# Kernel tuning notes

Hardware: AMD Instinct MI355X
Metric: run time of the kernel (lower is better)

The kernel has to match this reference:

```python
import jax, jax.numpy as jnp
import numpy as np

B, N, I, H = 4, 325, 64, 128
LN_EPS = 1e-5

def setup_inputs() -> dict:
    key = jax.random.key(0)
    ks = jax.random.split(key, 20)
    x = jax.random.normal(ks[0], (B, N, I), dtype=jnp.float32)
    # sparse binary adjacency with self-loops (as the module masks adj == 0)
    a = (jax.random.uniform(ks[1], (B, N, N)) < 0.05).astype(jnp.float32)
    adj = jnp.maximum(a, jnp.eye(N, dtype=jnp.float32)[None])
    h = jax.random.normal(ks[2], (B, N, H), dtype=jnp.float32)
    c = jax.random.normal(ks[3], (B, N, H), dtype=jnp.float32)
    def glorot(k, shape):
        fan_in, fan_out = shape[-1], shape[0]
        s = jnp.sqrt(2.0 / (fan_in + fan_out)).astype(jnp.float32)
        return jax.random.normal(k, shape, dtype=jnp.float32) * s
    params = {
        'W_ih': glorot(ks[4], (4 * H, I)),
        'W_hh': glorot(ks[5], (4 * H, H)),
        'b_ih': jnp.zeros((4 * H,), jnp.float32),
        'b_hh': jnp.zeros((4 * H,), jnp.float32),
        'gc_w': glorot(ks[6], (H, H)),
        'gc_b': jnp.zeros((H,), jnp.float32),
        'Ws_w': glorot(ks[7], (H, H)),
        'Ws_b': jnp.zeros((H,), jnp.float32),
        'Wt_w': glorot(ks[8], (H, H)),
        'Wt_b': jnp.zeros((H,), jnp.float32),
        'v': glorot(ks[9], (H, 1)),
        'ln_g': jnp.ones((H,), jnp.float32),
        'ln_b': jnp.zeros((H,), jnp.float32),
        'comb_w': glorot(ks[10], (H, 2 * H)),
        'comb_b': jnp.zeros((H,), jnp.float32),
    }
    return {'x': x, 'adj': adj, 'h': h, 'c': c, **params}


def reference(x, adj, h, c, W_ih, W_hh, b_ih, b_hh, gc_w, gc_b,
              Ws_w, Ws_b, Wt_w, Wt_b, v, ln_g, ln_b, comb_w, comb_b):
    # --- LSTMCell applied per node (PyTorch gate order: i, f, g, o) ---
    gates = (jnp.einsum('bni,gi->bng', x, W_ih) + b_ih
             + jnp.einsum('bnh,gh->bng', h, W_hh) + b_hh)  # [B,N,4H]
    i_g, f_g, g_g, o_g = jnp.split(gates, 4, axis=-1)
    c_lstm = jax.nn.sigmoid(f_g) * c + jax.nn.sigmoid(i_g) * jnp.tanh(g_g)
    h_lstm = jax.nn.sigmoid(o_g) * jnp.tanh(c_lstm)  # [B,N,H]
    # --- Graph convolution: adj @ (h W) + b ---
    support = jnp.einsum('bnh,ho->bno', h_lstm, gc_w)
    h_graph = jnp.einsum('bnm,bmo->bno', adj, support) + gc_b
    # --- Spatial attention (tanh-additive, adjacency-masked softmax) ---
    s = jnp.einsum('bnh,oh->bno', h_graph, Ws_w) + Ws_b  # W_s(x)
    t = jnp.einsum('bnh,oh->bno', h_graph, Wt_w) + Wt_b  # W_t(x)
    # scores[b,i,j] = tanh(s[b,i] + t[b,j]) @ v ; big [B,N,N,H] intermediate
    scores = jnp.einsum('bijh,h->bij',
                        jnp.tanh(s[:, :, None, :] + t[:, None, :, :]),
                        v[:, 0])
    scores = jnp.where(adj == 0, -1e9, scores)
    attn = jax.nn.softmax(scores, axis=-1)
    context = jnp.einsum('bij,bjh->bih', attn, h_graph)
    # --- LayerNorm ---
    mu = jnp.mean(context, axis=-1, keepdims=True)
    var = jnp.var(context, axis=-1, keepdims=True)
    h_att = ln_g * (context - mu) * jax.lax.rsqrt(var + LN_EPS) + ln_b
    # --- Combine ---
    h_comb = jnp.concatenate([h_lstm, h_att], axis=-1)
    h_new = jnp.einsum('bnk,ok->bno', h_comb, comb_w) + comb_b
    return (h_new, c_lstm)
```

## Files before the change

kernel.cpp:

```cpp
#include <hip/hip_runtime.h>

#define B_ 4
#define N_ 325
#define I_ 64
#define H_ 128
#define NODES (B_ * N_)
#define NZMAX 64
#define NBLK (NODES / 4)

typedef unsigned short u16;
typedef unsigned int u32;

__device__ __align__(16) float g_WT   [192 * 512];
__device__ __align__(16) float g_gcw  [128 * 128];
__device__ __align__(16) float g_WsT  [128 * 128];
__device__ __align__(16) float g_WtT  [128 * 128];
__device__ __align__(16) float g_combT[256 * 128];
__device__ float g_bias[512];
__device__ float g_svec[896];

__device__ __align__(16) float g_support[(size_t)NODES * H_];
__device__ __align__(16) float g_h_graph[(size_t)NODES * H_];
__device__ __align__(16) float g_s_buf  [(size_t)NODES * H_];
__device__ __align__(16) float g_t_buf  [(size_t)NODES * H_];
__device__ __align__(16) float g_hl     [(size_t)NODES * H_];
__device__ u16 g_nz [(size_t)NODES * NZMAX];
__device__ int g_nzc[NODES];

__device__ __forceinline__ float bf2f(u16 u) { return __uint_as_float(((u32)u) << 16); }
__device__ __forceinline__ u16 f2bf(float f) {
    u32 u = __float_as_uint(f);
    u += 0x7fffu + ((u >> 16) & 1u);
    return (u16)(u >> 16);
}
__device__ __forceinline__ float ldin(const void* p, size_t i, int f32) {
    return f32 ? ((const float*)p)[i] : bf2f(((const u16*)p)[i]);
}
__device__ __forceinline__ void stout(void* p, size_t i, float v, int f32) {
    if (f32) ((float*)p)[i] = v; else ((u16*)p)[i] = f2bf(v);
}
__device__ __forceinline__ float fast_rcp(float x) { return __builtin_amdgcn_rcpf(x); }
__device__ __forceinline__ float sigm(float x) { return fast_rcp(1.f + __expf(-x)); }
__device__ __forceinline__ float tanh_f(float x) {
    x = fminf(15.f, fmaxf(-15.f, x));
    float e = __expf(2.f * x);
    return (e - 1.f) * fast_rcp(e + 1.f);
}
__device__ __forceinline__ int probe_f32(const void* adj) {
    return ((((const u32*)adj)[0] & 0xFFFFu) != 0x3F80u) ? 1 : 0;
}

__global__ __launch_bounds__(256) void k0_prep(
    const void* __restrict__ W_ih, const void* __restrict__ W_hh,
    const void* __restrict__ b_ih, const void* __restrict__ b_hh,
    const void* __restrict__ gc_w, const void* __restrict__ gc_b,
    const void* __restrict__ Ws_w, const void* __restrict__ Ws_b,
    const void* __restrict__ Wt_w, const void* __restrict__ Wt_b,
    const void* __restrict__ vvec, const void* __restrict__ ln_g,
    const void* __restrict__ ln_b, const void* __restrict__ comb_w,
    const void* __restrict__ comb_b, const void* __restrict__ adj)
{
    const int f32 = probe_f32(adj);
    const int tid = blockIdx.x * 256 + threadIdx.x;
    const int nth = gridDim.x * 256;
    const int TOT = 98304 + 16384 * 3 + 32768 + 512 + 896;
    for (int e = tid; e < TOT; e += nth) {
        int i = e;
        if (i < 98304) {
            const int k = i >> 9, g = i & 511;
            g_WT[i] = (k < 64) ? ldin(W_ih, (size_t)g * 64 + k, f32)
                               : ldin(W_hh, (size_t)g * 128 + (k - 64), f32);
            continue;
        }
        i -= 98304;
        if (i < 16384) { g_gcw[i] = ldin(gc_w, i, f32); continue; }
        i -= 16384;
        if (i < 16384) {
            const int k = i >> 7, o = i & 127;
            g_WsT[i] = ldin(Ws_w, (size_t)o * 128 + k, f32);
            continue;
        }
        i -= 16384;
        if (i < 16384) {
            const int k = i >> 7, o = i & 127;
            g_WtT[i] = ldin(Wt_w, (size_t)o * 128 + k, f32);
            continue;
        }
        i -= 16384;
        if (i < 32768) {
            const int k = i >> 7, o = i & 127;
            g_combT[i] = ldin(comb_w, (size_t)o * 256 + k, f32);
            continue;
        }
        i -= 32768;
        if (i < 512) { g_bias[i] = ldin(b_ih, i, f32) + ldin(b_hh, i, f32); continue; }
        i -= 512;
        {
            const int seg = i >> 7, k = i & 127;
            const void* src = (seg == 0) ? gc_b : (seg == 1) ? Ws_b : (seg == 2) ? Wt_b :
                              (seg == 3) ? vvec : (seg == 4) ? ln_g : (seg == 5) ? ln_b : comb_b;
            g_svec[i] = ldin(src, k, f32);
        }
    }
}

__global__ __launch_bounds__(512) void k1_lstm(
    const void* __restrict__ x, const void* __restrict__ h, const void* __restrict__ c,
    const void* __restrict__ adj, void* __restrict__ out)
{
    const int f32 = probe_f32(adj);
    __shared__ __align__(16) float4 xh4[192];
    __shared__ __align__(16) float4 Gt4[512];
    __shared__ __align__(16) float4 hl4[128];
    const int node0 = blockIdx.x * 4;
    const int t = threadIdx.x;

    for (int e = t; e < 768; e += 512) {
        const int n = e / 192, k = e % 192;
        const int node = node0 + n;
        ((float*)&xh4[k])[n] = (k < 64) ? ldin(x, (size_t)node * 64 + k, f32)
                                        : ldin(h, (size_t)node * 128 + (k - 64), f32);
    }
    __syncthreads();

    {
        const int g = t;
        float a0 = 0.f, a1 = 0.f, a2 = 0.f, a3 = 0.f;
        #pragma unroll 8
        for (int k = 0; k < 192; ++k) {
            const float wv = g_WT[(size_t)k * 512 + g];
            const float4 xv = xh4[k];
            a0 = fmaf(xv.x, wv, a0); a1 = fmaf(xv.y, wv, a1);
            a2 = fmaf(xv.z, wv, a2); a3 = fmaf(xv.w, wv, a3);
        }
        const float bias = g_bias[g];
        Gt4[g] = make_float4(a0 + bias, a1 + bias, a2 + bias, a3 + bias);
    }
    __syncthreads();

    {
        const int n = t >> 7, hh = t & 127;
        const int node = node0 + n;
        float ig = ((const float*)&Gt4[hh])[n];
        float fg = ((const float*)&Gt4[128 + hh])[n];
        float gv = ((const float*)&Gt4[256 + hh])[n];
        float og = ((const float*)&Gt4[384 + hh])[n];
        float cl = sigm(fg) * ldin(c, (size_t)node * 128 + hh, f32) + sigm(ig) * tanh_f(gv);
        float hv = sigm(og) * tanh_f(cl);
        stout(out, (size_t)(NODES * H_) + (size_t)node * 128 + hh, cl, f32);
        g_hl[(size_t)node * 128 + hh] = hv;
        ((float*)&hl4[hh])[n] = hv;
    }
    __syncthreads();

    {
        const int o = t & 127, n = t >> 7;
        float acc = 0.f;
        #pragma unroll 8
        for (int k = 0; k < 128; ++k)
            acc = fmaf(((const float*)&hl4[k])[n], g_gcw[(size_t)k * 128 + o], acc);
        g_support[(size_t)(node0 + n) * 128 + o] = acc;
    }
}

__global__ __launch_bounds__(256) void k2_graph(const void* __restrict__ adj)
{
    const int f32 = probe_f32(adj);
    __shared__ __align__(16) float4 hg4[128];
    __shared__ u16 nzi[4][NZMAX];
    __shared__ float nzv[4][NZMAX];
    __shared__ int cnt[4];
    const int node0 = blockIdx.x * 4;
    const int t = threadIdx.x;
    const int lane = t & 63, w = t >> 6;

    if (t < 4) cnt[t] = 0;
    __syncthreads();
    for (int j = lane; j < N_; j += 64) {
        float a = ldin(adj, (size_t)(node0 + w) * N_ + j, f32);
        if (a != 0.f) {
            int p = atomicAdd(&cnt[w], 1);
            if (p < NZMAX) { nzi[w][p] = (u16)j; nzv[w][p] = a; }
        }
    }
    __syncthreads();
    if (t < 4) g_nzc[node0 + t] = min(cnt[t], NZMAX);
    #pragma unroll
    for (int n = 0; n < 4; ++n) {
        const int cnn = min(cnt[n], NZMAX);
        for (int p = t; p < cnn; p += 256) g_nz[(size_t)(node0 + n) * NZMAX + p] = nzi[n][p];
    }

    const int o = t & 127;
    const float gb = g_svec[o];
    #pragma unroll
    for (int ps = 0; ps < 2; ++ps) {
        const int n = (t >> 7) + 2 * ps;
        const int node = node0 + n;
        const int bn = node / N_;
        const int cnn = min(cnt[n], NZMAX);
        float acc = gb;
        for (int p = 0; p < cnn; ++p)
            acc = fmaf(nzv[n][p], g_support[((size_t)bn * N_ + nzi[n][p]) * 128 + o], acc);
        g_h_graph[(size_t)node * 128 + o] = acc;
        ((float*)&hg4[o])[n] = acc;
    }
    __syncthreads();

    {
        const int which = t >> 7;
        const float* WT = which ? g_WtT : g_WsT;
        const float bias = g_svec[128 + which * 128 + o];
        float a0 = 0.f, a1 = 0.f, a2 = 0.f, a3 = 0.f;
        #pragma unroll 8
        for (int k = 0; k < 128; ++k) {
            const float wv = WT[(size_t)k * 128 + o];
            const float4 hv = hg4[k];
            a0 = fmaf(hv.x, wv, a0); a1 = fmaf(hv.y, wv, a1);
            a2 = fmaf(hv.z, wv, a2); a3 = fmaf(hv.w, wv, a3);
        }
        float* dst = which ? g_t_buf : g_s_buf;
        dst[(size_t)(node0 + 0) * 128 + o] = a0 + bias;
        dst[(size_t)(node0 + 1) * 128 + o] = a1 + bias;
        dst[(size_t)(node0 + 2) * 128 + o] = a2 + bias;
        dst[(size_t)(node0 + 3) * 128 + o] = a3 + bias;
    }
}

__global__ __launch_bounds__(256) void k3_attn(
    const void* __restrict__ adj, void* __restrict__ out)
{
    const int f32 = probe_f32(adj);
    __shared__ __align__(16) float4 comb4[256];
    __shared__ float s_i[4][H_];
    __shared__ float red[4][H_];
    __shared__ float nzs[4][NZMAX];
    __shared__ u16 nzi[4][NZMAX];
    __shared__ float part[2][4][H_];
    __shared__ float mu_[4], rstd_[4], smv[4];
    __shared__ int cnt[4];
    const int node0 = blockIdx.x * 4;
    const int t = threadIdx.x;
    const int lane = t & 63, w = t >> 6;

    if (t < 4) cnt[t] = g_nzc[node0 + t];
    for (int e = t; e < 512; e += 256) {
        const int n = e >> 7, k = e & 127;
        const int node = node0 + n;
        s_i[n][k] = g_s_buf[(size_t)node * 128 + k];
        ((float*)&comb4[k])[n] = g_hl[(size_t)node * 128 + k];
    }
    __syncthreads();
    #pragma unroll
    for (int n = 0; n < 4; ++n)
        for (int p = t; p < cnt[n]; p += 256) nzi[n][p] = g_nz[(size_t)(node0 + n) * NZMAX + p];
    __syncthreads();

    {
        const int bn = (node0 + w) / N_;
        const int cn = cnt[w];
        const float v0 = g_svec[384 + lane], v1 = g_svec[384 + 64 + lane];
        const float si0 = s_i[w][lane], si1 = s_i[w][lane + 64];
        for (int p = 0; p < cn; ++p) {
            const float* tj = g_t_buf + ((size_t)bn * N_ + nzi[w][p]) * 128;
            float a = v0 * tanh_f(si0 + tj[lane]) + v1 * tanh_f(si1 + tj[lane + 64]);
            #pragma unroll
            for (int off = 32; off > 0; off >>= 1) a += __shfl_xor(a, off);
            if (lane == 0) nzs[w][p] = a;
        }
    }
    __syncthreads();

    if (t < 4) {
        const int cn = cnt[t];
        float m = -1e30f;
        for (int p = 0; p < cn; ++p) m = fmaxf(m, nzs[t][p]);
        float ssum = 0.f;
        for (int p = 0; p < cn; ++p) { float e = __expf(nzs[t][p] - m); nzs[t][p] = e; ssum += e; }
        smv[t] = fast_rcp(ssum);
    }
    __syncthreads();

    const int o = t & 127;
    #pragma unroll
    for (int ps = 0; ps < 2; ++ps) {
        const int n = (t >> 7) + 2 * ps;
        const int bn = (node0 + n) / N_;
        const int cn = cnt[n];
        float acc = 0.f;
        for (int p = 0; p < cn; ++p)
            acc = fmaf(nzs[n][p], g_h_graph[((size_t)bn * N_ + nzi[n][p]) * 128 + o], acc);
        red[n][o] = acc * smv[n];
    }
    __syncthreads();

    {
        float x0 = red[w][lane], x1 = red[w][lane + 64];
        float sm = x0 + x1, sq = x0 * x0 + x1 * x1;
        #pragma unroll
        for (int off = 32; off > 0; off >>= 1) {
            sm += __shfl_xor(sm, off);
            sq += __shfl_xor(sq, off);
        }
        if (lane == 0) {
            float mu = sm * (1.f / H_);
            float var = fmaxf(sq * (1.f / H_) - mu * mu, 0.f);
            mu_[w] = mu;
            rstd_[w] = __builtin_amdgcn_rsqf(var + 1e-5f);
        }
    }
    __syncthreads();
    for (int e = t; e < 512; e += 256) {
        const int n = e >> 7, k = e & 127;
        float xn = (red[n][k] - mu_[n]) * rstd_[n];
        ((float*)&comb4[128 + k])[n] = g_svec[512 + k] * xn + g_svec[640 + k];
    }
    __syncthreads();

    {
        const int half = t >> 7;
        float a0 = 0.f, a1 = 0.f, a2 = 0.f, a3 = 0.f;
        const int k0 = half * 128;
        #pragma unroll 8
        for (int kk = 0; kk < 128; ++kk) {
            const int k = k0 + kk;
            const float wv = g_combT[(size_t)k * 128 + o];
            const float4 cv = comb4[k];
            a0 = fmaf(cv.x, wv, a0); a1 = fmaf(cv.y, wv, a1);
            a2 = fmaf(cv.z, wv, a2); a3 = fmaf(cv.w, wv, a3);
        }
        part[half][0][o] = a0; part[half][1][o] = a1;
        part[half][2][o] = a2; part[half][3][o] = a3;
    }
    __syncthreads();
    for (int e = t; e < 512; e += 256) {
        const int n = e >> 7, k = e & 127;
        stout(out, (size_t)(node0 + n) * 128 + k,
              part[0][n][k] + part[1][n][k] + g_svec[768 + k], f32);
    }
}

extern "C" void kernel_launch(void* const* d_in, const int* in_sizes, int n_in,
                              void* d_out, int out_size, void* d_ws, size_t ws_size,
                              hipStream_t stream)
{
    (void)in_sizes; (void)n_in; (void)out_size; (void)d_ws; (void)ws_size;
    const void* x      = d_in[0];
    const void* adj    = d_in[1];
    const void* h      = d_in[2];
    const void* c      = d_in[3];
    const void* W_ih   = d_in[4];
    const void* W_hh   = d_in[5];
    const void* b_ih   = d_in[6];
    const void* b_hh   = d_in[7];
    const void* gc_w   = d_in[8];
    const void* gc_b   = d_in[9];
    const void* Ws_w   = d_in[10];
    const void* Ws_b   = d_in[11];
    const void* Wt_w   = d_in[12];
    const void* Wt_b   = d_in[13];
    const void* vvec   = d_in[14];
    const void* ln_g   = d_in[15];
    const void* ln_b   = d_in[16];
    const void* comb_w = d_in[17];
    const void* comb_b = d_in[18];

    k0_prep <<<256, 256, 0, stream>>>(W_ih, W_hh, b_ih, b_hh, gc_w, gc_b,
                                      Ws_w, Ws_b, Wt_w, Wt_b, vvec, ln_g, ln_b,
                                      comb_w, comb_b, adj);
    k1_lstm <<<NBLK, 512, 0, stream>>>(x, h, c, adj, d_out);
    k2_graph<<<NBLK, 256, 0, stream>>>(adj);
    k3_attn <<<NBLK, 256, 0, stream>>>(adj, d_out);
}
```

Measured before the change: 152.2 us.

## Move adjacency scan into LSTM kernel and widen graph/attention kernels to 512 threads

The adjacency nonzero extraction moves from k2 into k1, so k1 now writes the column indices, weights and counts to global memory. k2 and k3 now launch 512 threads per block. They split the K dimension of the Ws/Wt and combine matmuls into halves or quarters and reduce the partial sums through shared memory, and k3 spreads attention scoring over two waves per node. The goal is more parallelism per block and shorter serial loops. The cost is extra global traffic for the nonzero weights, more shared memory, and additional synchronisation.

```diff
diff --git a/kernel.cpp b/kernel.cpp
--- a/kernel.cpp
+++ b/kernel.cpp
@@ -21,11 +21,12 @@
 
 __device__ __align__(16) float g_support[(size_t)NODES * H_];
 __device__ __align__(16) float g_h_graph[(size_t)NODES * H_];
+__device__ __align__(16) float g_t_buf  [(size_t)NODES * H_];
 __device__ __align__(16) float g_s_buf  [(size_t)NODES * H_];
-__device__ __align__(16) float g_t_buf  [(size_t)NODES * H_];
 __device__ __align__(16) float g_hl     [(size_t)NODES * H_];
-__device__ u16 g_nz [(size_t)NODES * NZMAX];
-__device__ int g_nzc[NODES];
+__device__ u16   g_nz [(size_t)NODES * NZMAX];
+__device__ float g_nzw[(size_t)NODES * NZMAX];
+__device__ int   g_nzc[NODES];
 
 __device__ __forceinline__ float bf2f(u16 u) { return __uint_as_float(((u32)u) << 16); }
 __device__ __forceinline__ u16 f2bf(float f) {
@@ -112,9 +113,13 @@
     __shared__ __align__(16) float4 xh4[192];
     __shared__ __align__(16) float4 Gt4[512];
     __shared__ __align__(16) float4 hl4[128];
+    __shared__ u16 nzi[4][NZMAX];
+    __shared__ float nzv[4][NZMAX];
+    __shared__ int cnt[4];
     const int node0 = blockIdx.x * 4;
     const int t = threadIdx.x;
 
+    if (t < 4) cnt[t] = 0;
     for (int e = t; e < 768; e += 512) {
         const int n = e / 192, k = e % 192;
         const int node = node0 + n;
@@ -151,8 +156,28 @@
         g_hl[(size_t)node * 128 + hh] = hv;
         ((float*)&hl4[hh])[n] = hv;
     }
-    __syncthreads();
-
+    {
+        const int n = t >> 7, jj = t & 127;
+        const size_t row = (size_t)(node0 + n) * N_;
+        for (int j = jj; j < N_; j += 128) {
+            float a = ldin(adj, row + j, f32);
+            if (a != 0.f) {
+                int p = atomicAdd(&cnt[n], 1);
+                if (p < NZMAX) { nzi[n][p] = (u16)j; nzv[n][p] = a; }
+            }
+        }
+    }
+    __syncthreads();
+
+    if (t < 4) g_nzc[node0 + t] = min(cnt[t], NZMAX);
+    #pragma unroll
+    for (int n = 0; n < 4; ++n) {
+        const int cnn = min(cnt[n], NZMAX);
+        for (int p = t; p < cnn; p += 512) {
+            g_nz [(size_t)(node0 + n) * NZMAX + p] = nzi[n][p];
+            g_nzw[(size_t)(node0 + n) * NZMAX + p] = nzv[n][p];
+        }
+    }
     {
         const int o = t & 127, n = t >> 7;
         float acc = 0.f;
@@ -163,43 +188,35 @@
     }
 }
 
-__global__ __launch_bounds__(256) void k2_graph(const void* __restrict__ adj)
+__global__ __launch_bounds__(512) void k2_graph(const void* __restrict__ adj)
 {
-    const int f32 = probe_f32(adj);
+    (void)adj;
     __shared__ __align__(16) float4 hg4[128];
     __shared__ u16 nzi[4][NZMAX];
     __shared__ float nzv[4][NZMAX];
     __shared__ int cnt[4];
+    __shared__ float part[4][4][H_];
     const int node0 = blockIdx.x * 4;
     const int t = threadIdx.x;
-    const int lane = t & 63, w = t >> 6;
-
-    if (t < 4) cnt[t] = 0;
-    __syncthreads();
-    for (int j = lane; j < N_; j += 64) {
-        float a = ldin(adj, (size_t)(node0 + w) * N_ + j, f32);
-        if (a != 0.f) {
-            int p = atomicAdd(&cnt[w], 1);
-            if (p < NZMAX) { nzi[w][p] = (u16)j; nzv[w][p] = a; }
-        }
-    }
-    __syncthreads();
-    if (t < 4) g_nzc[node0 + t] = min(cnt[t], NZMAX);
+
+    if (t < 4) cnt[t] = g_nzc[node0 + t];
+    __syncthreads();
     #pragma unroll
     for (int n = 0; n < 4; ++n) {
-        const int cnn = min(cnt[n], NZMAX);
-        for (int p = t; p < cnn; p += 256) g_nz[(size_t)(node0 + n) * NZMAX + p] = nzi[n][p];
-    }
-
-    const int o = t & 127;
-    const float gb = g_svec[o];
-    #pragma unroll
-    for (int ps = 0; ps < 2; ++ps) {
-        const int n = (t >> 7) + 2 * ps;
+        const int cnn = cnt[n];
+        for (int p = t; p < cnn; p += 512) {
+            nzi[n][p] = g_nz [(size_t)(node0 + n) * NZMAX + p];
+            nzv[n][p] = g_nzw[(size_t)(node0 + n) * NZMAX + p];
+        }
+    }
+    __syncthreads();
+
+    {
+        const int n = t >> 7, o = t & 127;
         const int node = node0 + n;
         const int bn = node / N_;
-        const int cnn = min(cnt[n], NZMAX);
-        float acc = gb;
+        const int cnn = cnt[n];
+        float acc = g_svec[o];
         for (int p = 0; p < cnn; ++p)
             acc = fmaf(nzv[n][p], g_support[((size_t)bn * N_ + nzi[n][p]) * 128 + o], acc);
         g_h_graph[(size_t)node * 128 + o] = acc;
@@ -208,35 +225,45 @@
     __syncthreads();
 
     {
-        const int which = t >> 7;
+        const int o = t & 127;
+        const int which = (t >> 7) & 1;
+        const int half  = t >> 8;
         const float* WT = which ? g_WtT : g_WsT;
-        const float bias = g_svec[128 + which * 128 + o];
+        const int k0 = half * 64;
         float a0 = 0.f, a1 = 0.f, a2 = 0.f, a3 = 0.f;
         #pragma unroll 8
-        for (int k = 0; k < 128; ++k) {
+        for (int kk = 0; kk < 64; ++kk) {
+            const int k = k0 + kk;
             const float wv = WT[(size_t)k * 128 + o];
             const float4 hv = hg4[k];
             a0 = fmaf(hv.x, wv, a0); a1 = fmaf(hv.y, wv, a1);
             a2 = fmaf(hv.z, wv, a2); a3 = fmaf(hv.w, wv, a3);
         }
+        const int s = which * 2 + half;
+        part[s][0][o] = a0; part[s][1][o] = a1;
+        part[s][2][o] = a2; part[s][3][o] = a3;
+    }
+    __syncthreads();
+    for (int e = t; e < 1024; e += 512) {
+        const int which = e >> 9, n = (e >> 7) & 3, o = e & 127;
+        const float vsum = part[which * 2][n][o] + part[which * 2 + 1][n][o]
+                         + g_svec[128 + which * 128 + o];
         float* dst = which ? g_t_buf : g_s_buf;
-        dst[(size_t)(node0 + 0) * 128 + o] = a0 + bias;
-        dst[(size_t)(node0 + 1) * 128 + o] = a1 + bias;
-        dst[(size_t)(node0 + 2) * 128 + o] = a2 + bias;
-        dst[(size_t)(node0 + 3) * 128 + o] = a3 + bias;
-    }
-}
-
-__global__ __launch_bounds__(256) void k3_attn(
+        dst[(size_t)(node0 + n) * 128 + o] = vsum;
+    }
+}
+
+__global__ __launch_bounds__(512) void k3_attn(
     const void* __restrict__ adj, void* __restrict__ out)
 {
     const int f32 = probe_f32(adj);
-    __shared__ __align__(16) float4 comb4[256];
+    __shared__ __align__(16) float4 hl4[128];
+    __shared__ __align__(16) float4 att4[128];
     __shared__ float s_i[4][H_];
     __shared__ float red[4][H_];
     __shared__ float nzs[4][NZMAX];
     __shared__ u16 nzi[4][NZMAX];
-    __shared__ float part[2][4][H_];
+    __shared__ float part[4][4][H_];
     __shared__ float mu_[4], rstd_[4], smv[4];
     __shared__ int cnt[4];
     const int node0 = blockIdx.x * 4;
@@ -244,33 +271,34 @@
     const int lane = t & 63, w = t >> 6;
 
     if (t < 4) cnt[t] = g_nzc[node0 + t];
-    for (int e = t; e < 512; e += 256) {
+    for (int e = t; e < 512; e += 512) {
         const int n = e >> 7, k = e & 127;
         const int node = node0 + n;
         s_i[n][k] = g_s_buf[(size_t)node * 128 + k];
-        ((float*)&comb4[k])[n] = g_hl[(size_t)node * 128 + k];
+        ((float*)&hl4[k])[n] = g_hl[(size_t)node * 128 + k];
     }
     __syncthreads();
     #pragma unroll
     for (int n = 0; n < 4; ++n)
-        for (int p = t; p < cnt[n]; p += 256) nzi[n][p] = g_nz[(size_t)(node0 + n) * NZMAX + p];
-    __syncthreads();
-
-    {
-        const int bn = (node0 + w) / N_;
-        const int cn = cnt[w];
+        for (int p = t; p < cnt[n]; p += 512)
+            nzi[n][p] = g_nz[(size_t)(node0 + n) * NZMAX + p];
+    __syncthreads();
+
+    {
+        const int n = w & 3;
+        const int bn = (node0 + n) / N_;
+        const int cn = cnt[n];
         const float v0 = g_svec[384 + lane], v1 = g_svec[384 + 64 + lane];
-        const float si0 = s_i[w][lane], si1 = s_i[w][lane + 64];
-        for (int p = 0; p < cn; ++p) {
-            const float* tj = g_t_buf + ((size_t)bn * N_ + nzi[w][p]) * 128;
+        const float si0 = s_i[n][lane], si1 = s_i[n][lane + 64];
+        for (int p = (w >> 2); p < cn; p += 2) {
+            const float* tj = g_t_buf + ((size_t)bn * N_ + nzi[n][p]) * 128;
             float a = v0 * tanh_f(si0 + tj[lane]) + v1 * tanh_f(si1 + tj[lane + 64]);
             #pragma unroll
             for (int off = 32; off > 0; off >>= 1) a += __shfl_xor(a, off);
-            if (lane == 0) nzs[w][p] = a;
-        }
-    }
-    __syncthreads();
-
+            if (lane == 0) nzs[n][p] = a;
+        }
+    }
+    __syncthreads();
     if (t < 4) {
         const int cn = cnt[t];
         float m = -1e30f;
@@ -281,10 +309,8 @@
     }
     __syncthreads();
 
-    const int o = t & 127;
-    #pragma unroll
-    for (int ps = 0; ps < 2; ++ps) {
-        const int n = (t >> 7) + 2 * ps;
+    {
+        const int n = t >> 7, o = t & 127;
         const int bn = (node0 + n) / N_;
         const int cn = cnt[n];
         float acc = 0.f;
@@ -294,7 +320,7 @@
     }
     __syncthreads();
 
-    {
+    if (w < 4) {
         float x0 = red[w][lane], x1 = red[w][lane + 64];
         float sm = x0 + x1, sq = x0 * x0 + x1 * x1;
         #pragma unroll
@@ -310,33 +336,35 @@
         }
     }
     __syncthreads();
-    for (int e = t; e < 512; e += 256) {
-        const int n = e >> 7, k = e & 127;
+    {
+        const int n = t >> 7, k = t & 127;
         float xn = (red[n][k] - mu_[n]) * rstd_[n];
-        ((float*)&comb4[128 + k])[n] = g_svec[512 + k] * xn + g_svec[640 + k];
-    }
-    __syncthreads();
-
-    {
-        const int half = t >> 7;
+        ((float*)&att4[k])[n] = g_svec[512 + k] * xn + g_svec[640 + k];
+    }
+    __syncthreads();
+
+    {
+        const int o = t & 127, q = t >> 7;
+        const float4* src = (q < 2) ? hl4 : att4;
+        const int kb = (q < 2) ? q * 64 : (q - 2) * 64;
+        const int k0 = q * 64;
         float a0 = 0.f, a1 = 0.f, a2 = 0.f, a3 = 0.f;
-        const int k0 = half * 128;
         #pragma unroll 8
-        for (int kk = 0; kk < 128; ++kk) {
-            const int k = k0 + kk;
-            const float wv = g_combT[(size_t)k * 128 + o];
-            const float4 cv = comb4[k];
+        for (int kk = 0; kk < 64; ++kk) {
+            const float wv = g_combT[(size_t)(k0 + kk) * 128 + o];
+            const float4 cv = src[kb + kk];
             a0 = fmaf(cv.x, wv, a0); a1 = fmaf(cv.y, wv, a1);
             a2 = fmaf(cv.z, wv, a2); a3 = fmaf(cv.w, wv, a3);
         }
-        part[half][0][o] = a0; part[half][1][o] = a1;
-        part[half][2][o] = a2; part[half][3][o] = a3;
-    }
-    __syncthreads();
-    for (int e = t; e < 512; e += 256) {
-        const int n = e >> 7, k = e & 127;
+        part[q][0][o] = a0; part[q][1][o] = a1;
+        part[q][2][o] = a2; part[q][3][o] = a3;
+    }
+    __syncthreads();
+    {
+        const int n = t >> 7, k = t & 127;
         stout(out, (size_t)(node0 + n) * 128 + k,
-              part[0][n][k] + part[1][n][k] + g_svec[768 + k], f32);
+              part[0][n][k] + part[1][n][k] + part[2][n][k] + part[3][n][k]
+              + g_svec[768 + k], f32);
     }
 }
 
@@ -369,6 +397,6 @@
                                       Ws_w, Ws_b, Wt_w, Wt_b, vvec, ln_g, ln_b,
                                       comb_w, comb_b, adj);
     k1_lstm <<<NBLK, 512, 0, stream>>>(x, h, c, adj, d_out);
-    k2_graph<<<NBLK, 256, 0, stream>>>(adj);
-    k3_attn <<<NBLK, 256, 0, stream>>>(adj, d_out);
-}
+    k2_graph<<<NBLK, 512, 0, stream>>>(adj);
+    k3_attn <<<NBLK, 512, 0, stream>>>(adj, d_out);
+}
```

Result: faster. 141.1 us (-7.3%).

## Process six nodes per block and move adjacency compaction into LSTM kernel

Applied to the files above, without the earlier changes.

Raises nodes per block from 4 to 6 (217 blocks), so each weight load from global memory is reused across more nodes in the LSTM, graph-conv, Ws/Wt and combine GEMVs. The adjacency scan and nonzero compaction move from k2 into k1, and the edge weights are now stored to global for k2 to reuse. The prep kernel's transpose writes are reordered to read inputs coalesced. The tail block needs bounds checks, and fewer blocks lowers the number of concurrent workgroups on the GPU.

```diff
diff --git a/kernel.cpp b/kernel.cpp
--- a/kernel.cpp
+++ b/kernel.cpp
@@ -6,7 +6,8 @@
 #define H_ 128
 #define NODES (B_ * N_)
 #define NZMAX 64
-#define NBLK (NODES / 4)
+#define NB 6
+#define NBLK6 217
 
 typedef unsigned short u16;
 typedef unsigned int u32;
@@ -21,11 +22,12 @@
 
 __device__ __align__(16) float g_support[(size_t)NODES * H_];
 __device__ __align__(16) float g_h_graph[(size_t)NODES * H_];
+__device__ __align__(16) float g_t_buf  [(size_t)NODES * H_];
 __device__ __align__(16) float g_s_buf  [(size_t)NODES * H_];
-__device__ __align__(16) float g_t_buf  [(size_t)NODES * H_];
 __device__ __align__(16) float g_hl     [(size_t)NODES * H_];
-__device__ u16 g_nz [(size_t)NODES * NZMAX];
-__device__ int g_nzc[NODES];
+__device__ u16   g_nz [(size_t)NODES * NZMAX];
+__device__ float g_nzw[(size_t)NODES * NZMAX];
+__device__ int   g_nzc[NODES];
 
 __device__ __forceinline__ float bf2f(u16 u) { return __uint_as_float(((u32)u) << 16); }
 __device__ __forceinline__ u16 f2bf(float f) {
@@ -67,29 +69,30 @@
     for (int e = tid; e < TOT; e += nth) {
         int i = e;
         if (i < 98304) {
-            const int k = i >> 9, g = i & 511;
-            g_WT[i] = (k < 64) ? ldin(W_ih, (size_t)g * 64 + k, f32)
-                               : ldin(W_hh, (size_t)g * 128 + (k - 64), f32);
+            const int g = i / 192, kk = i % 192;
+            const float v = (kk < 64) ? ldin(W_ih, (size_t)g * 64 + kk, f32)
+                                      : ldin(W_hh, (size_t)g * 128 + (kk - 64), f32);
+            g_WT[(size_t)kk * 512 + g] = v;
             continue;
         }
         i -= 98304;
         if (i < 16384) { g_gcw[i] = ldin(gc_w, i, f32); continue; }
         i -= 16384;
         if (i < 16384) {
-            const int k = i >> 7, o = i & 127;
-            g_WsT[i] = ldin(Ws_w, (size_t)o * 128 + k, f32);
+            const int o = i >> 7, k = i & 127;
+            g_WsT[(size_t)k * 128 + o] = ldin(Ws_w, (size_t)o * 128 + k, f32);
             continue;
         }
         i -= 16384;
         if (i < 16384) {
-            const int k = i >> 7, o = i & 127;
-            g_WtT[i] = ldin(Wt_w, (size_t)o * 128 + k, f32);
+            const int o = i >> 7, k = i & 127;
+            g_WtT[(size_t)k * 128 + o] = ldin(Wt_w, (size_t)o * 128 + k, f32);
             continue;
         }
         i -= 16384;
         if (i < 32768) {
-            const int k = i >> 7, o = i & 127;
-            g_combT[i] = ldin(comb_w, (size_t)o * 256 + k, f32);
+            const int o = i >> 8, k = i & 255;
+            g_combT[(size_t)k * 128 + o] = ldin(comb_w, (size_t)o * 256 + k, f32);
             continue;
         }
         i -= 32768;
@@ -104,126 +107,172 @@
     }
 }
 
-__global__ __launch_bounds__(512) void k1_lstm(
+__global__ __launch_bounds__(256) void k1_lstm(
     const void* __restrict__ x, const void* __restrict__ h, const void* __restrict__ c,
     const void* __restrict__ adj, void* __restrict__ out)
 {
     const int f32 = probe_f32(adj);
-    __shared__ __align__(16) float4 xh4[192];
-    __shared__ __align__(16) float4 Gt4[512];
-    __shared__ __align__(16) float4 hl4[128];
-    const int node0 = blockIdx.x * 4;
-    const int t = threadIdx.x;
-
-    for (int e = t; e < 768; e += 512) {
-        const int n = e / 192, k = e % 192;
-        const int node = node0 + n;
-        ((float*)&xh4[k])[n] = (k < 64) ? ldin(x, (size_t)node * 64 + k, f32)
-                                        : ldin(h, (size_t)node * 128 + (k - 64), f32);
-    }
-    __syncthreads();
-
-    {
-        const int g = t;
-        float a0 = 0.f, a1 = 0.f, a2 = 0.f, a3 = 0.f;
-        #pragma unroll 8
-        for (int k = 0; k < 192; ++k) {
-            const float wv = g_WT[(size_t)k * 512 + g];
-            const float4 xv = xh4[k];
-            a0 = fmaf(xv.x, wv, a0); a1 = fmaf(xv.y, wv, a1);
-            a2 = fmaf(xv.z, wv, a2); a3 = fmaf(xv.w, wv, a3);
-        }
-        const float bias = g_bias[g];
-        Gt4[g] = make_float4(a0 + bias, a1 + bias, a2 + bias, a3 + bias);
-    }
-    __syncthreads();
-
-    {
-        const int n = t >> 7, hh = t & 127;
-        const int node = node0 + n;
-        float ig = ((const float*)&Gt4[hh])[n];
-        float fg = ((const float*)&Gt4[128 + hh])[n];
-        float gv = ((const float*)&Gt4[256 + hh])[n];
-        float og = ((const float*)&Gt4[384 + hh])[n];
-        float cl = sigm(fg) * ldin(c, (size_t)node * 128 + hh, f32) + sigm(ig) * tanh_f(gv);
-        float hv = sigm(og) * tanh_f(cl);
-        stout(out, (size_t)(NODES * H_) + (size_t)node * 128 + hh, cl, f32);
-        g_hl[(size_t)node * 128 + hh] = hv;
-        ((float*)&hl4[hh])[n] = hv;
-    }
-    __syncthreads();
-
-    {
-        const int o = t & 127, n = t >> 7;
-        float acc = 0.f;
-        #pragma unroll 8
-        for (int k = 0; k < 128; ++k)
-            acc = fmaf(((const float*)&hl4[k])[n], g_gcw[(size_t)k * 128 + o], acc);
-        g_support[(size_t)(node0 + n) * 128 + o] = acc;
-    }
-}
-
-__global__ __launch_bounds__(256) void k2_graph(const void* __restrict__ adj)
-{
-    const int f32 = probe_f32(adj);
-    __shared__ __align__(16) float4 hg4[128];
-    __shared__ u16 nzi[4][NZMAX];
-    __shared__ float nzv[4][NZMAX];
-    __shared__ int cnt[4];
-    const int node0 = blockIdx.x * 4;
+    __shared__ __align__(16) float xh[192][8];
+    __shared__ float Gt[512][NB];
+    __shared__ float hl[128][NB];
+    __shared__ u16 nzi[NB][NZMAX];
+    __shared__ float nzv[NB][NZMAX];
+    __shared__ int cnt[NB];
+    const int node0 = blockIdx.x * NB;
     const int t = threadIdx.x;
     const int lane = t & 63, w = t >> 6;
 
-    if (t < 4) cnt[t] = 0;
-    __syncthreads();
-    for (int j = lane; j < N_; j += 64) {
-        float a = ldin(adj, (size_t)(node0 + w) * N_ + j, f32);
-        if (a != 0.f) {
-            int p = atomicAdd(&cnt[w], 1);
-            if (p < NZMAX) { nzi[w][p] = (u16)j; nzv[w][p] = a; }
-        }
-    }
-    __syncthreads();
-    if (t < 4) g_nzc[node0 + t] = min(cnt[t], NZMAX);
+    if (t < NB) cnt[t] = 0;
+    for (int e = t; e < 192 * NB; e += 256) {
+        const int k = e % 192, n = e / 192;
+        const int node = node0 + n;
+        float v = 0.f;
+        if (node < NODES)
+            v = (k < 64) ? ldin(x, (size_t)node * 64 + k, f32)
+                         : ldin(h, (size_t)node * 128 + (k - 64), f32);
+        xh[k][n] = v;
+    }
+    __syncthreads();
+
+    {
+        float a0[NB] = {0,0,0,0,0,0};
+        float a1[NB] = {0,0,0,0,0,0};
+        #pragma unroll 4
+        for (int k = 0; k < 192; ++k) {
+            const float4 x4 = *(const float4*)&xh[k][0];
+            const float2 x2 = *(const float2*)&xh[k][4];
+            const float w0 = g_WT[(size_t)k * 512 + t];
+            const float w1 = g_WT[(size_t)k * 512 + t + 256];
+            a0[0] = fmaf(x4.x, w0, a0[0]); a1[0] = fmaf(x4.x, w1, a1[0]);
+            a0[1] = fmaf(x4.y, w0, a0[1]); a1[1] = fmaf(x4.y, w1, a1[1]);
+            a0[2] = fmaf(x4.z, w0, a0[2]); a1[2] = fmaf(x4.z, w1, a1[2]);
+            a0[3] = fmaf(x4.w, w0, a0[3]); a1[3] = fmaf(x4.w, w1, a1[3]);
+            a0[4] = fmaf(x2.x, w0, a0[4]); a1[4] = fmaf(x2.x, w1, a1[4]);
+            a0[5] = fmaf(x2.y, w0, a0[5]); a1[5] = fmaf(x2.y, w1, a1[5]);
+        }
+        const float b0 = g_bias[t], b1 = g_bias[t + 256];
+        #pragma unroll
+        for (int n = 0; n < NB; ++n) {
+            Gt[t][n]       = a0[n] + b0;
+            Gt[t + 256][n] = a1[n] + b1;
+        }
+    }
+    __syncthreads();
+
+    for (int e = t; e < 128 * NB; e += 256) {
+        const int k = e & 127, n = e >> 7;
+        const int node = node0 + n;
+        const float ig = Gt[k][n];
+        const float fg = Gt[128 + k][n];
+        const float gg = Gt[256 + k][n];
+        const float og = Gt[384 + k][n];
+        const float cp = (node < NODES) ? ldin(c, (size_t)node * 128 + k, f32) : 0.f;
+        const float cl = sigm(fg) * cp + sigm(ig) * tanh_f(gg);
+        const float hv = sigm(og) * tanh_f(cl);
+        if (node < NODES) {
+            stout(out, (size_t)(NODES * H_) + (size_t)node * 128 + k, cl, f32);
+            g_hl[(size_t)node * 128 + k] = hv;
+        }
+        hl[k][n] = hv;
+    }
+    for (int rr = w; rr < NB; rr += 4) {
+        const int node = node0 + rr;
+        if (node < NODES) {
+            const size_t row = (size_t)node * N_;
+            for (int j = lane; j < N_; j += 64) {
+                const float a = ldin(adj, row + j, f32);
+                if (a != 0.f) {
+                    const int p = atomicAdd(&cnt[rr], 1);
+                    if (p < NZMAX) { nzi[rr][p] = (u16)j; nzv[rr][p] = a; }
+                }
+            }
+        }
+    }
+    __syncthreads();
+
+    if (t < NB && node0 + t < NODES) g_nzc[node0 + t] = min(cnt[t], NZMAX);
     #pragma unroll
-    for (int n = 0; n < 4; ++n) {
+    for (int n = 0; n < NB; ++n) {
+        if (node0 + n >= NODES) continue;
         const int cnn = min(cnt[n], NZMAX);
-        for (int p = t; p < cnn; p += 256) g_nz[(size_t)(node0 + n) * NZMAX + p] = nzi[n][p];
-    }
-
-    const int o = t & 127;
-    const float gb = g_svec[o];
+        for (int p = t; p < cnn; p += 256) {
+            g_nz [(size_t)(node0 + n) * NZMAX + p] = nzi[n][p];
+            g_nzw[(size_t)(node0 + n) * NZMAX + p] = nzv[n][p];
+        }
+    }
+    {
+        const int o = t & 127, n2 = t >> 7;
+        #pragma unroll
+        for (int np = 0; np < 3; ++np) {
+            const int n = n2 + 2 * np;
+            const int node = node0 + n;
+            float acc = 0.f;
+            #pragma unroll 8
+            for (int k = 0; k < 128; ++k)
+                acc = fmaf(hl[k][n], g_gcw[(size_t)k * 128 + o], acc);
+            if (node < NODES) g_support[(size_t)node * 128 + o] = acc;
+        }
+    }
+}
+
+__global__ __launch_bounds__(256) void k2_graph()
+{
+    __shared__ __align__(16) float hg[128][8];
+    __shared__ u16 nzi[NB][NZMAX];
+    __shared__ float nzv[NB][NZMAX];
+    __shared__ int cnt[NB];
+    const int node0 = blockIdx.x * NB;
+    const int t = threadIdx.x;
+
+    if (t < NB) cnt[t] = (node0 + t < NODES) ? g_nzc[node0 + t] : 0;
+    __syncthreads();
     #pragma unroll
-    for (int ps = 0; ps < 2; ++ps) {
-        const int n = (t >> 7) + 2 * ps;
-        const int node = node0 + n;
-        const int bn = node / N_;
-        const int cnn = min(cnt[n], NZMAX);
-        float acc = gb;
-        for (int p = 0; p < cnn; ++p)
-            acc = fmaf(nzv[n][p], g_support[((size_t)bn * N_ + nzi[n][p]) * 128 + o], acc);
-        g_h_graph[(size_t)node * 128 + o] = acc;
-        ((float*)&hg4[o])[n] = acc;
-    }
-    __syncthreads();
-
-    {
-        const int which = t >> 7;
+    for (int n = 0; n < NB; ++n) {
+        const int cnn = cnt[n];
+        for (int p = t; p < cnn; p += 256) {
+            nzi[n][p] = g_nz [(size_t)(node0 + n) * NZMAX + p];
+            nzv[n][p] = g_nzw[(size_t)(node0 + n) * NZMAX + p];
+        }
+    }
+    __syncthreads();
+
+    {
+        const int o = t & 127, n2 = t >> 7;
+        #pragma unroll
+        for (int np = 0; np < 3; ++np) {
+            const int n = n2 + 2 * np;
+            const int node = node0 + n;
+            const int bn = node / N_;
+            const int cnn = cnt[n];
+            float acc = g_svec[o];
+            for (int p = 0; p < cnn; ++p)
+                acc = fmaf(nzv[n][p], g_support[((size_t)bn * N_ + nzi[n][p]) * 128 + o], acc);
+            if (node < NODES) g_h_graph[(size_t)node * 128 + o] = acc;
+            hg[o][n] = acc;
+        }
+    }
+    __syncthreads();
+
+    {
+        const int o = t & 127, which = t >> 7;
         const float* WT = which ? g_WtT : g_WsT;
         const float bias = g_svec[128 + which * 128 + o];
-        float a0 = 0.f, a1 = 0.f, a2 = 0.f, a3 = 0.f;
-        #pragma unroll 8
+        float a[NB] = {0,0,0,0,0,0};
+        #pragma unroll 4
         for (int k = 0; k < 128; ++k) {
             const float wv = WT[(size_t)k * 128 + o];
-            const float4 hv = hg4[k];
-            a0 = fmaf(hv.x, wv, a0); a1 = fmaf(hv.y, wv, a1);
-            a2 = fmaf(hv.z, wv, a2); a3 = fmaf(hv.w, wv, a3);
+            const float4 h4 = *(const float4*)&hg[k][0];
+            const float2 h2 = *(const float2*)&hg[k][4];
+            a[0] = fmaf(h4.x, wv, a[0]); a[1] = fmaf(h4.y, wv, a[1]);
+            a[2] = fmaf(h4.z, wv, a[2]); a[3] = fmaf(h4.w, wv, a[3]);
+            a[4] = fmaf(h2.x, wv, a[4]); a[5] = fmaf(h2.y, wv, a[5]);
         }
         float* dst = which ? g_t_buf : g_s_buf;
-        dst[(size_t)(node0 + 0) * 128 + o] = a0 + bias;
-        dst[(size_t)(node0 + 1) * 128 + o] = a1 + bias;
-        dst[(size_t)(node0 + 2) * 128 + o] = a2 + bias;
-        dst[(size_t)(node0 + 3) * 128 + o] = a3 + bias;
+        #pragma unroll
+        for (int n = 0; n < NB; ++n) {
+            const int node = node0 + n;
+            if (node < NODES) dst[(size_t)node * 128 + o] = a[n] + bias;
+        }
     }
 }
 
@@ -231,47 +280,53 @@
     const void* __restrict__ adj, void* __restrict__ out)
 {
     const int f32 = probe_f32(adj);
-    __shared__ __align__(16) float4 comb4[256];
-    __shared__ float s_i[4][H_];
-    __shared__ float red[4][H_];
-    __shared__ float nzs[4][NZMAX];
-    __shared__ u16 nzi[4][NZMAX];
-    __shared__ float part[2][4][H_];
-    __shared__ float mu_[4], rstd_[4], smv[4];
-    __shared__ int cnt[4];
-    const int node0 = blockIdx.x * 4;
+    __shared__ float s_i[NB][H_];
+    __shared__ __align__(16) float hlc[128][8];
+    __shared__ __align__(16) float att[128][8];
+    __shared__ float red[NB][H_];
+    __shared__ float nzs[NB][NZMAX];
+    __shared__ u16 nzi[NB][NZMAX];
+    __shared__ float part[2][NB][H_];
+    __shared__ float mu_[NB], rstd_[NB], smv[NB];
+    __shared__ int cnt[NB];
+    const int node0 = blockIdx.x * NB;
     const int t = threadIdx.x;
     const int lane = t & 63, w = t >> 6;
 
-    if (t < 4) cnt[t] = g_nzc[node0 + t];
-    for (int e = t; e < 512; e += 256) {
-        const int n = e >> 7, k = e & 127;
+    if (t < NB) cnt[t] = (node0 + t < NODES) ? g_nzc[node0 + t] : 0;
+    for (int e = t; e < 128 * NB; e += 256) {
+        const int k = e & 127, n = e >> 7;
         const int node = node0 + n;
-        s_i[n][k] = g_s_buf[(size_t)node * 128 + k];
-        ((float*)&comb4[k])[n] = g_hl[(size_t)node * 128 + k];
+        float sv = 0.f, hv = 0.f;
+        if (node < NODES) {
+            sv = g_s_buf[(size_t)node * 128 + k];
+            hv = g_hl  [(size_t)node * 128 + k];
+        }
+        s_i[n][k] = sv;
+        hlc[k][n] = hv;
     }
     __syncthreads();
     #pragma unroll
-    for (int n = 0; n < 4; ++n)
-        for (int p = t; p < cnt[n]; p += 256) nzi[n][p] = g_nz[(size_t)(node0 + n) * NZMAX + p];
-    __syncthreads();
-
-    {
-        const int bn = (node0 + w) / N_;
-        const int cn = cnt[w];
+    for (int n = 0; n < NB; ++n)
+        for (int p = t; p < cnt[n]; p += 256)
+            nzi[n][p] = g_nz[(size_t)(node0 + n) * NZMAX + p];
+    __syncthreads();
+
+    for (int nn = w; nn < NB; nn += 4) {
+        const int bn = (node0 + nn) / N_;
+        const int cn = cnt[nn];
         const float v0 = g_svec[384 + lane], v1 = g_svec[384 + 64 + lane];
-        const float si0 = s_i[w][lane], si1 = s_i[w][lane + 64];
+        const float si0 = s_i[nn][lane], si1 = s_i[nn][lane + 64];
         for (int p = 0; p < cn; ++p) {
-            const float* tj = g_t_buf + ((size_t)bn * N_ + nzi[w][p]) * 128;
+            const float* tj = g_t_buf + ((size_t)bn * N_ + nzi[nn][p]) * 128;
             float a = v0 * tanh_f(si0 + tj[lane]) + v1 * tanh_f(si1 + tj[lane + 64]);
             #pragma unroll
             for (int off = 32; off > 0; off >>= 1) a += __shfl_xor(a, off);
-            if (lane == 0) nzs[w][p] = a;
-        }
-    }
-    __syncthreads();
-
-    if (t < 4) {
+            if (lane == 0) nzs[nn][p] = a;
+        }
+    }
+    __syncthreads();
+    if (t < NB) {
         const int cn = cnt[t];
         float m = -1e30f;
         for (int p = 0; p < cn; ++p) m = fmaxf(m, nzs[t][p]);
@@ -281,21 +336,23 @@
     }
     __syncthreads();
 
-    const int o = t & 127;
-    #pragma unroll
-    for (int ps = 0; ps < 2; ++ps) {
-        const int n = (t >> 7) + 2 * ps;
-        const int bn = (node0 + n) / N_;
-        const int cn = cnt[n];
-        float acc = 0.f;
-        for (int p = 0; p < cn; ++p)
-            acc = fmaf(nzs[n][p], g_h_graph[((size_t)bn * N_ + nzi[n][p]) * 128 + o], acc);
-        red[n][o] = acc * smv[n];
-    }
-    __syncthreads();
-
-    {
-        float x0 = red[w][lane], x1 = red[w][lane + 64];
+    {
+        const int o = t & 127, n2 = t >> 7;
+        #pragma unroll
+        for (int np = 0; np < 3; ++np) {
+            const int n = n2 + 2 * np;
+            const int bn = (node0 + n) / N_;
+            const int cn = cnt[n];
+            float acc = 0.f;
+            for (int p = 0; p < cn; ++p)
+                acc = fmaf(nzs[n][p], g_h_graph[((size_t)bn * N_ + nzi[n][p]) * 128 + o], acc);
+            red[n][o] = acc * smv[n];
+        }
+    }
+    __syncthreads();
+
+    for (int nn = w; nn < NB; nn += 4) {
+        float x0 = red[nn][lane], x1 = red[nn][lane + 64];
         float sm = x0 + x1, sq = x0 * x0 + x1 * x1;
         #pragma unroll
         for (int off = 32; off > 0; off >>= 1) {
@@ -303,40 +360,44 @@
             sq += __shfl_xor(sq, off);
         }
         if (lane == 0) {
-            float mu = sm * (1.f / H_);
-            float var = fmaxf(sq * (1.f / H_) - mu * mu, 0.f);
-            mu_[w] = mu;
-            rstd_[w] = __builtin_amdgcn_rsqf(var + 1e-5f);
-        }
-    }
-    __syncthreads();
-    for (int e = t; e < 512; e += 256) {
-        const int n = e >> 7, k = e & 127;
-        float xn = (red[n][k] - mu_[n]) * rstd_[n];
-        ((float*)&comb4[128 + k])[n] = g_svec[512 + k] * xn + g_svec[640 + k];
-    }
-    __syncthreads();
-
-    {
-        const int half = t >> 7;
-        float a0 = 0.f, a1 = 0.f, a2 = 0.f, a3 = 0.f;
-        const int k0 = half * 128;
-        #pragma unroll 8
+            const float mu = sm * (1.f / H_);
+            const float var = fmaxf(sq * (1.f / H_) - mu * mu, 0.f);
+            mu_[nn] = mu;
+            rstd_[nn] = __builtin_amdgcn_rsqf(var + 1e-5f);
+        }
+    }
+    __syncthreads();
+    for (int e = t; e < 128 * NB; e += 256) {
+        const int k = e & 127, n = e >> 7;
+        const float xn = (red[n][k] - mu_[n]) * rstd_[n];
+        att[k][n] = g_svec[512 + k] * xn + g_svec[640 + k];
+    }
+    __syncthreads();
+
+    {
+        const int o = t & 127, half = t >> 7;
+        float a[NB] = {0,0,0,0,0,0};
+        #pragma unroll 4
         for (int kk = 0; kk < 128; ++kk) {
-            const int k = k0 + kk;
+            const int k = half * 128 + kk;
             const float wv = g_combT[(size_t)k * 128 + o];
-            const float4 cv = comb4[k];
-            a0 = fmaf(cv.x, wv, a0); a1 = fmaf(cv.y, wv, a1);
-            a2 = fmaf(cv.z, wv, a2); a3 = fmaf(cv.w, wv, a3);
-        }
-        part[half][0][o] = a0; part[half][1][o] = a1;
-        part[half][2][o] = a2; part[half][3][o] = a3;
-    }
-    __syncthreads();
-    for (int e = t; e < 512; e += 256) {
-        const int n = e >> 7, k = e & 127;
-        stout(out, (size_t)(node0 + n) * 128 + k,
-              part[0][n][k] + part[1][n][k] + g_svec[768 + k], f32);
+            const float* src = half ? &att[kk][0] : &hlc[kk][0];
+            const float4 c4 = *(const float4*)src;
+            const float2 c2 = *(const float2*)(src + 4);
+            a[0] = fmaf(c4.x, wv, a[0]); a[1] = fmaf(c4.y, wv, a[1]);
+            a[2] = fmaf(c4.z, wv, a[2]); a[3] = fmaf(c4.w, wv, a[3]);
+            a[4] = fmaf(c2.x, wv, a[4]); a[5] = fmaf(c2.y, wv, a[5]);
+        }
+        #pragma unroll
+        for (int n = 0; n < NB; ++n) part[half][n][o] = a[n];
+    }
+    __syncthreads();
+    for (int e = t; e < 128 * NB; e += 256) {
+        const int k = e & 127, n = e >> 7;
+        const int node = node0 + n;
+        if (node < NODES)
+            stout(out, (size_t)node * 128 + k,
+                  part[0][n][k] + part[1][n][k] + g_svec[768 + k], f32);
     }
 }
 
@@ -368,7 +429,7 @@
     k0_prep <<<256, 256, 0, stream>>>(W_ih, W_hh, b_ih, b_hh, gc_w, gc_b,
                                       Ws_w, Ws_b, Wt_w, Wt_b, vvec, ln_g, ln_b,
                                       comb_w, comb_b, adj);
-    k1_lstm <<<NBLK, 512, 0, stream>>>(x, h, c, adj, d_out);
-    k2_graph<<<NBLK, 256, 0, stream>>>(adj);
-    k3_attn <<<NBLK, 256, 0, stream>>>(adj, d_out);
-}
+    k1_lstm <<<NBLK6, 256, 0, stream>>>(x, h, c, adj, d_out);
+    k2_graph<<<NBLK6, 256, 0, stream>>>();
+    k3_attn <<<NBLK6, 256, 0, stream>>>(adj, d_out);
+}
```

After: 184.4 us. 21.2% more time.
